# Kernel optimization log

Measured on AMD Instinct MI355X. Metric: run time of the kernel, lower is better.

Reference implementation:

```python
import jax, jax.numpy as jnp
import numpy as np

DELTA = 5.0          # weight on positive BCE term
R = 0.01             # hard-negative fraction
M, N = 4096, 16384   # batch rows, memory-bank size
NUM_HARD = int(R * (N - 1))  # int(r * neg_count); each row has exactly 1 positive


def setup_inputs() -> dict:
    key = jax.random.key(0)
    k1, k2 = jax.random.split(key)
    inputs = jax.random.normal(k1, (M, N), dtype=jnp.float32)
    targets = jax.random.randint(k2, (M,), 0, N)
    return {"inputs": inputs, "targets": targets}


def reference(inputs, targets):
    m, n = inputs.shape
    rows = jnp.arange(m)
    # positive logit per row (one-hot scatter => exactly one positive)
    pos = inputs[rows, targets]                          # [m]
    # BCE with logits, target=1: softplus(-x); mean over the single positive
    l_pos = jax.nn.softplus(-pos)                        # [m]
    # exclude positive from negatives by sinking it to -inf, then hard top-k
    neg_inf = jnp.finfo(inputs.dtype).min
    masked = inputs.at[rows, targets].set(neg_inf)       # [m, n]
    hard_neg, _ = jax.lax.top_k(masked, NUM_HARD)        # [m, NUM_HARD]
    # BCE with logits, target=0: softplus(x); mean over hard negatives
    l_neg = jnp.mean(jax.nn.softplus(hard_neg), axis=1)  # [m]
    return jnp.mean(DELTA * l_pos + l_neg)
```

## Files before the change

### kernel.cpp

```cpp
#include <hip/hip_runtime.h>
#include <stdint.h>

#define M_ROWS 4096
#define N_COLS 16384
#define K_HARD 163
#define DELTA_W 5.0f
#define THREADS 1024
#define NWAVES  16
#define RPB     8
#define GRID    (M_ROWS / RPB)
#define THRESH  2.0f
#define KEY_MIN 0xC0000000u
#define SEGC    64

__device__ __forceinline__ uint32_t f2key(float x) {
    uint32_t u = __float_as_uint(x);
    return u ^ (uint32_t)(((int32_t)u >> 31) | 0x80000000u);
}
__device__ __forceinline__ float key2f(uint32_t k) {
    uint32_t u = (k & 0x80000000u) ? (k & 0x7fffffffu) : ~k;
    return __uint_as_float(u);
}
__device__ __forceinline__ float softplus_f(float x) {
    return fmaxf(x, 0.0f) + log1pf(__expf(-fabsf(x)));
}

__device__ __forceinline__ void wscan1024(const uint32_t* h, int lane, int K,
                                          int& pivot, int& krem) {
    int c[16]; int S = 0;
#pragma unroll
    for (int q = 0; q < 16; ++q) { c[q] = (int)h[lane * 16 + q]; S += c[q]; }
    int suf = S;
    for (int off = 1; off < 64; off <<= 1) {
        int y = __shfl_down(suf, off);
        if (lane + off < 64) suf += y;
    }
    int run = suf - S;
    int enc = 0;
#pragma unroll
    for (int b = 15; b >= 0; --b) {
        const int cc = c[b];
        if (run < K && run + cc >= K) enc = ((lane * 16 + b + 1) << 8) | (K - run);
        run += cc;
    }
    for (int off = 1; off < 64; off <<= 1) enc = max(enc, __shfl_xor(enc, off));
    pivot = (enc >> 8) - 1; krem = enc & 255;
}

__device__ float wave_fallback(const float4* row4, int tgt, uint32_t* hrow, int lane) {
    uint32_t pref = 0; int K = K_HARD;
    for (int pass = 0; pass < 3; ++pass) {
        const int shift = 22 - 10 * pass;
        for (int q = 0; q < 16; ++q) hrow[q * 64 + lane] = 0;
        for (int s2 = 0; s2 < 64; ++s2) {
            const float4 v = row4[s2 * 64 + lane];
            const int j0 = (s2 * 64 + lane) * 4;
            const float e[4] = {v.x, v.y, v.z, v.w};
#pragma unroll
            for (int q = 0; q < 4; ++q) {
                if (j0 + q == tgt) continue;
                const uint32_t k = f2key(e[q]);
                if (pass == 0 || (k >> (shift + 10)) == pref)
                    atomicAdd(&hrow[(k >> shift) & 1023u], 1u);
            }
        }
        int pv, kr; wscan1024(hrow, lane, K, pv, kr);
        pref = (pref << 10) | (uint32_t)pv; K = kr;
    }
    for (int q = 0; q < 16; ++q) hrow[q * 64 + lane] = 0;
    for (int s2 = 0; s2 < 64; ++s2) {
        const float4 v = row4[s2 * 64 + lane];
        const int j0 = (s2 * 64 + lane) * 4;
        const float e[4] = {v.x, v.y, v.z, v.w};
#pragma unroll
        for (int q = 0; q < 4; ++q) {
            if (j0 + q == tgt) continue;
            const uint32_t k = f2key(e[q]);
            if ((k >> 2) == pref) atomicAdd(&hrow[k & 3u], 1u);
        }
    }
    int piv = 0, tie = K;
    { int run = 0;
      for (int b2 = 3; b2 >= 0; --b2) {
          const int cc = (int)hrow[b2];
          if (run < K && run + cc >= K) { piv = b2; tie = K - run; }
          run += cc;
      } }
    const uint32_t T = (pref << 2) | (uint32_t)piv;
    float sum = 0.0f;
    for (int s2 = 0; s2 < 64; ++s2) {
        const float4 v = row4[s2 * 64 + lane];
        const int j0 = (s2 * 64 + lane) * 4;
        const float e[4] = {v.x, v.y, v.z, v.w};
#pragma unroll
        for (int q = 0; q < 4; ++q) {
            if (j0 + q == tgt) continue;
            const uint32_t k = f2key(e[q]);
            if (k > T) sum += softplus_f(e[q]);
        }
    }
    for (int off = 32; off; off >>= 1) sum += __shfl_down(sum, off);
    if (lane == 0) sum += (float)tie * softplus_f(key2f(T));
    return sum;
}

__global__ __launch_bounds__(THREADS, 8) void mmcl_main(
        const float* __restrict__ inputs,
        const int* __restrict__ targets,
        float* __restrict__ partial) {
    __shared__ uint32_t s_seg[NWAVES][RPB][SEGC];
    __shared__ uint32_t s_hist[RPB][1024];
    __shared__ int s_cnt[NWAVES][RPB];

    const int b = blockIdx.x;
    const int t = threadIdx.x;
    const int lane = t & 63;
    const int w = t >> 6;
    const float4* in4 = (const float4*)inputs;
    const int gbase = b * (RPB * 4096);

    for (int r = 0; r < RPB; ++r) {
        int wcount = 0;
#pragma unroll
        for (int ii = 0; ii < 4; ++ii) {
            const float4 v = in4[gbase + (r * 4 + ii) * 1024 + t];
            const float e[4] = {v.x, v.y, v.z, v.w};
            const int n = (v.x >= THRESH) + (v.y >= THRESH) +
                          (v.z >= THRESH) + (v.w >= THRESH);
            int inc = n;
            for (int off = 1; off < 64; off <<= 1) {
                int y = __shfl_up(inc, off);
                if (lane >= off) inc += y;
            }
            int base = wcount + inc - n;
            int j = 0;
#pragma unroll
            for (int q = 0; q < 4; ++q) {
                if (e[q] >= THRESH) {
                    const int d = base + j;
                    if (d < SEGC) s_seg[w][r][d] = f2key(e[q]);
                    ++j;
                }
            }
            wcount += __shfl(inc, 63);
        }
        if (lane == 0) s_cnt[w][r] = wcount;
    }
    __syncthreads();

    if (w < RPB) {
        const int r = w;
        const int grow = b * RPB + r;
        const int tgt = targets[grow];
        const float pos = inputs[(size_t)grow * N_COLS + tgt];
        const uint32_t tkey = f2key(pos);
        const float4* row4 = (const float4*)(inputs + (size_t)grow * N_COLS);
        uint32_t* hrow = &s_hist[r][0];

        bool fb = false;
        for (int s = 0; s < NWAVES; ++s) fb |= ((int)s_cnt[s][r] > SEGC);

        if (!fb && pos >= THRESH) {
            bool removed = false;
            for (int s = 0; s < NWAVES && !removed; ++s) {
                const int cc = (int)s_cnt[s][r];
                const uint32_t k = (lane < cc) ? s_seg[s][r][lane] : (tkey + 1u);
                const unsigned long long m = __ballot(lane < cc && k == tkey);
                if (m) {
                    const int f = __ffsll(m) - 1;
                    if (lane == 0) {
                        s_seg[s][r][f] = s_seg[s][r][cc - 1];
                        s_cnt[s][r] = cc - 1;
                    }
                    removed = true;
                }
            }
        }
        int ncand = 0;
        for (int s = 0; s < NWAVES; ++s) ncand += (int)s_cnt[s][r];
        if (ncand < K_HARD) fb = true;

        float sum;
        if (!fb) {
            for (int q = 0; q < 16; ++q) hrow[q * 64 + lane] = 0;
            for (int s = 0; s < NWAVES; ++s) {
                const int cc = (int)s_cnt[s][r];
                if (lane < cc)
                    atomicAdd(&hrow[(s_seg[s][r][lane] - KEY_MIN) >> 20], 1u);
            }
            int p1, k1; wscan1024(hrow, lane, K_HARD, p1, k1);
            for (int q = 0; q < 16; ++q) hrow[q * 64 + lane] = 0;
            for (int s = 0; s < NWAVES; ++s) {
                const int cc = (int)s_cnt[s][r];
                if (lane < cc) {
                    const uint32_t d = s_seg[s][r][lane] - KEY_MIN;
                    if ((int)(d >> 20) == p1) atomicAdd(&hrow[(d >> 10) & 1023u], 1u);
                }
            }
            int p2, k2; wscan1024(hrow, lane, k1, p2, k2);
            const uint32_t pref2 = ((uint32_t)p1 << 10) | (uint32_t)p2;
            for (int q = 0; q < 16; ++q) hrow[q * 64 + lane] = 0;
            for (int s = 0; s < NWAVES; ++s) {
                const int cc = (int)s_cnt[s][r];
                if (lane < cc) {
                    const uint32_t d = s_seg[s][r][lane] - KEY_MIN;
                    if ((d >> 10) == pref2) atomicAdd(&hrow[d & 1023u], 1u);
                }
            }
            int p3, k3; wscan1024(hrow, lane, k2, p3, k3);
            const uint32_t T = KEY_MIN +
                (((uint32_t)p1 << 20) | ((uint32_t)p2 << 10) | (uint32_t)p3);
            sum = 0.0f;
            for (int s = 0; s < NWAVES; ++s) {
                const int cc = (int)s_cnt[s][r];
                if (lane < cc) {
                    const uint32_t k = s_seg[s][r][lane];
                    if (k > T) sum += softplus_f(key2f(k));
                }
            }
            for (int off = 32; off; off >>= 1) sum += __shfl_down(sum, off);
            if (lane == 0) sum += (float)k3 * softplus_f(key2f(T));
        } else {
            sum = wave_fallback(row4, tgt, hrow, lane);
        }

        if (lane == 0) {
            const float l_neg = sum / (float)K_HARD;
            partial[grow] = DELTA_W * softplus_f(-pos) + l_neg;
        }
    }
}

__global__ __launch_bounds__(256) void mmcl_reduce(
        const float* __restrict__ partial, float* __restrict__ out) {
    __shared__ float s_fw[4];
    const int t = threadIdx.x;
    float local = 0.0f;
    for (int i = t; i < M_ROWS; i += 256) local += partial[i];
    for (int off = 32; off; off >>= 1) local += __shfl_down(local, off);
    if ((t & 63) == 0) s_fw[t >> 6] = local;
    __syncthreads();
    if (t == 0)
        out[0] = (s_fw[0] + s_fw[1] + s_fw[2] + s_fw[3]) * (1.0f / (float)M_ROWS);
}

extern "C" void kernel_launch(void* const* d_in, const int* in_sizes, int n_in,
                              void* d_out, int out_size, void* d_ws, size_t ws_size,
                              hipStream_t stream) {
    const float* inputs = (const float*)d_in[0];
    const int* targets = (const int*)d_in[1];
    float* out = (float*)d_out;
    float* partial = (float*)d_ws;
    mmcl_main<<<GRID, THREADS, 0, stream>>>(inputs, targets, partial);
    mmcl_reduce<<<1, 256, 0, stream>>>(partial, out);
}
```

Baseline: 385.0 us.

## Split fused filter/select kernel into streaming filter pass and per-row select kernel

Replaces the single fused kernel, in which 1024-thread blocks filtered 8 rows into shared memory and then only 8 of 16 waves did the selection, with two kernels. The first is a grid-strided streaming kernel that compacts values above the threshold into per-64-lane global buckets of 24 slots, along with their counts. The second kernel gives each wave one row: it loads the bucketed keys into registers and runs the three-pass radix histogram select. This is meant to remove the idle-wave tail and raise occupancy of the bandwidth-bound pass. The cost is an extra kernel launch and a global write and read of the compacted candidates, plus more fallback risk because each segment now holds only 24 slots.

```diff
diff --git a/kernel.cpp b/kernel.cpp
--- a/kernel.cpp
+++ b/kernel.cpp
@@ -5,13 +5,13 @@
 #define N_COLS 16384
 #define K_HARD 163
 #define DELTA_W 5.0f
-#define THREADS 1024
-#define NWAVES  16
-#define RPB     8
-#define GRID    (M_ROWS / RPB)
 #define THRESH  2.0f
 #define KEY_MIN 0xC0000000u
-#define SEGC    64
+#define SLOTS   24
+#define WG      64
+#define GRID1   2048
+#define T1      256
+#define ITERS   32
 
 __device__ __forceinline__ uint32_t f2key(float x) {
     uint32_t u = __float_as_uint(x);
@@ -104,131 +104,119 @@
     return sum;
 }
 
-__global__ __launch_bounds__(THREADS, 8) void mmcl_main(
+__global__ __launch_bounds__(T1) void k1_front(
+        const float* __restrict__ inputs,
+        uint32_t* __restrict__ bucket,
+        int* __restrict__ cnts) {
+    const size_t flat = (size_t)blockIdx.x * T1 + threadIdx.x;
+    const int lane = threadIdx.x & 63;
+    const float4* in4 = (const float4*)inputs;
+#pragma unroll 4
+    for (int it = 0; it < ITERS; ++it) {
+        const size_t g = (size_t)it * ((size_t)GRID1 * T1) + flat;
+        const float4 v = in4[g];
+        const int row = (int)(g >> 12);
+        const int wg  = (int)((g >> 6) & 63);
+        const float e[4] = {v.x, v.y, v.z, v.w};
+        const int nc = (v.x >= THRESH) + (v.y >= THRESH) +
+                       (v.z >= THRESH) + (v.w >= THRESH);
+        int inc = nc;
+        for (int off = 1; off < 64; off <<= 1) {
+            int y = __shfl_up(inc, off);
+            if (lane >= off) inc += y;
+        }
+        uint32_t* seg = bucket + ((size_t)row * WG + wg) * SLOTS;
+        int d = inc - nc;
+#pragma unroll
+        for (int q = 0; q < 4; ++q) {
+            if (e[q] >= THRESH) {
+                if (d < SLOTS) seg[d] = f2key(e[q]);
+                ++d;
+            }
+        }
+        if (lane == 63) cnts[row * WG + wg] = inc;
+    }
+}
+
+__global__ __launch_bounds__(256) void k2_select(
         const float* __restrict__ inputs,
         const int* __restrict__ targets,
+        const uint32_t* __restrict__ bucket,
+        const int* __restrict__ cnts,
         float* __restrict__ partial) {
-    __shared__ uint32_t s_seg[NWAVES][RPB][SEGC];
-    __shared__ uint32_t s_hist[RPB][1024];
-    __shared__ int s_cnt[NWAVES][RPB];
-
-    const int b = blockIdx.x;
-    const int t = threadIdx.x;
-    const int lane = t & 63;
-    const int w = t >> 6;
-    const float4* in4 = (const float4*)inputs;
-    const int gbase = b * (RPB * 4096);
-
-    for (int r = 0; r < RPB; ++r) {
-        int wcount = 0;
-#pragma unroll
-        for (int ii = 0; ii < 4; ++ii) {
-            const float4 v = in4[gbase + (r * 4 + ii) * 1024 + t];
-            const float e[4] = {v.x, v.y, v.z, v.w};
-            const int n = (v.x >= THRESH) + (v.y >= THRESH) +
-                          (v.z >= THRESH) + (v.w >= THRESH);
-            int inc = n;
-            for (int off = 1; off < 64; off <<= 1) {
-                int y = __shfl_up(inc, off);
-                if (lane >= off) inc += y;
-            }
-            int base = wcount + inc - n;
-            int j = 0;
-#pragma unroll
-            for (int q = 0; q < 4; ++q) {
-                if (e[q] >= THRESH) {
-                    const int d = base + j;
-                    if (d < SEGC) s_seg[w][r][d] = f2key(e[q]);
-                    ++j;
+    __shared__ uint32_t sh[4][1024];
+    const int wid = threadIdx.x >> 6;
+    const int lane = threadIdx.x & 63;
+    const int row = blockIdx.x * 4 + wid;
+    const int tgt = targets[row];
+    const float pos = inputs[(size_t)row * N_COLS + tgt];
+    const float4* row4 = (const float4*)(inputs + (size_t)row * N_COLS);
+    uint32_t* hrow = sh[wid];
+
+    const int myc = cnts[row * WG + lane];
+    int mx = myc, sm = myc;
+    for (int off = 1; off < 64; off <<= 1) {
+        mx = max(mx, __shfl_xor(mx, off));
+        sm += __shfl_xor(sm, off);
+    }
+    bool fb = (mx > SLOTS);
+
+    uint32_t keys[SLOTS];
+    const int c = fb ? 0 : myc;
+    const uint32_t* seg = bucket + ((size_t)row * WG + lane) * SLOTS;
+#pragma unroll
+    for (int q = 0; q < SLOTS; ++q) keys[q] = (q < c) ? seg[q] : 0u;
+
+    int removed = 0;
+    if (!fb && pos >= THRESH) {
+        const uint32_t tkey = f2key(pos);
+        int q0 = SLOTS;
+        for (int q = SLOTS - 1; q >= 0; --q) if (keys[q] == tkey && q < c) q0 = q;
+        const unsigned long long m = __ballot(q0 < SLOTS);
+        if (m) {
+            const int leader = __ffsll(m) - 1;
+            if (lane == leader) keys[q0] = 0u;
+            removed = 1;
+        }
+        removed = __shfl(removed, 0);
+    }
+    const int ncand = sm - removed;
+    if (ncand < K_HARD) fb = true;
+
+    float sum;
+    if (!fb) {
+        uint32_t pref = 0; int K = K_HARD; int pv = 0, kr = K_HARD;
+#pragma unroll
+        for (int pass = 0; pass < 3; ++pass) {
+            const int shift = 20 - 10 * pass;
+            for (int q = 0; q < 16; ++q) hrow[q * 64 + lane] = 0;
+#pragma unroll
+            for (int q = 0; q < SLOTS; ++q) {
+                const uint32_t k = keys[q];
+                if (k >= KEY_MIN) {
+                    const uint32_t d = k - KEY_MIN;
+                    if (pass == 0 || (d >> (shift + 10)) == pref)
+                        atomicAdd(&hrow[(d >> shift) & 1023u], 1u);
                 }
             }
-            wcount += __shfl(inc, 63);
-        }
-        if (lane == 0) s_cnt[w][r] = wcount;
-    }
-    __syncthreads();
-
-    if (w < RPB) {
-        const int r = w;
-        const int grow = b * RPB + r;
-        const int tgt = targets[grow];
-        const float pos = inputs[(size_t)grow * N_COLS + tgt];
-        const uint32_t tkey = f2key(pos);
-        const float4* row4 = (const float4*)(inputs + (size_t)grow * N_COLS);
-        uint32_t* hrow = &s_hist[r][0];
-
-        bool fb = false;
-        for (int s = 0; s < NWAVES; ++s) fb |= ((int)s_cnt[s][r] > SEGC);
-
-        if (!fb && pos >= THRESH) {
-            bool removed = false;
-            for (int s = 0; s < NWAVES && !removed; ++s) {
-                const int cc = (int)s_cnt[s][r];
-                const uint32_t k = (lane < cc) ? s_seg[s][r][lane] : (tkey + 1u);
-                const unsigned long long m = __ballot(lane < cc && k == tkey);
-                if (m) {
-                    const int f = __ffsll(m) - 1;
-                    if (lane == 0) {
-                        s_seg[s][r][f] = s_seg[s][r][cc - 1];
-                        s_cnt[s][r] = cc - 1;
-                    }
-                    removed = true;
-                }
-            }
-        }
-        int ncand = 0;
-        for (int s = 0; s < NWAVES; ++s) ncand += (int)s_cnt[s][r];
-        if (ncand < K_HARD) fb = true;
-
-        float sum;
-        if (!fb) {
-            for (int q = 0; q < 16; ++q) hrow[q * 64 + lane] = 0;
-            for (int s = 0; s < NWAVES; ++s) {
-                const int cc = (int)s_cnt[s][r];
-                if (lane < cc)
-                    atomicAdd(&hrow[(s_seg[s][r][lane] - KEY_MIN) >> 20], 1u);
-            }
-            int p1, k1; wscan1024(hrow, lane, K_HARD, p1, k1);
-            for (int q = 0; q < 16; ++q) hrow[q * 64 + lane] = 0;
-            for (int s = 0; s < NWAVES; ++s) {
-                const int cc = (int)s_cnt[s][r];
-                if (lane < cc) {
-                    const uint32_t d = s_seg[s][r][lane] - KEY_MIN;
-                    if ((int)(d >> 20) == p1) atomicAdd(&hrow[(d >> 10) & 1023u], 1u);
-                }
-            }
-            int p2, k2; wscan1024(hrow, lane, k1, p2, k2);
-            const uint32_t pref2 = ((uint32_t)p1 << 10) | (uint32_t)p2;
-            for (int q = 0; q < 16; ++q) hrow[q * 64 + lane] = 0;
-            for (int s = 0; s < NWAVES; ++s) {
-                const int cc = (int)s_cnt[s][r];
-                if (lane < cc) {
-                    const uint32_t d = s_seg[s][r][lane] - KEY_MIN;
-                    if ((d >> 10) == pref2) atomicAdd(&hrow[d & 1023u], 1u);
-                }
-            }
-            int p3, k3; wscan1024(hrow, lane, k2, p3, k3);
-            const uint32_t T = KEY_MIN +
-                (((uint32_t)p1 << 20) | ((uint32_t)p2 << 10) | (uint32_t)p3);
-            sum = 0.0f;
-            for (int s = 0; s < NWAVES; ++s) {
-                const int cc = (int)s_cnt[s][r];
-                if (lane < cc) {
-                    const uint32_t k = s_seg[s][r][lane];
-                    if (k > T) sum += softplus_f(key2f(k));
-                }
-            }
-            for (int off = 32; off; off >>= 1) sum += __shfl_down(sum, off);
-            if (lane == 0) sum += (float)k3 * softplus_f(key2f(T));
-        } else {
-            sum = wave_fallback(row4, tgt, hrow, lane);
-        }
-
-        if (lane == 0) {
-            const float l_neg = sum / (float)K_HARD;
-            partial[grow] = DELTA_W * softplus_f(-pos) + l_neg;
-        }
-    }
+            wscan1024(hrow, lane, K, pv, kr);
+            pref = (pref << 10) | (uint32_t)pv; K = kr;
+        }
+        const uint32_t T = KEY_MIN + pref;
+        sum = 0.0f;
+#pragma unroll
+        for (int q = 0; q < SLOTS; ++q) {
+            const uint32_t k = keys[q];
+            if (k > T) sum += softplus_f(key2f(k));
+        }
+        for (int off = 32; off; off >>= 1) sum += __shfl_down(sum, off);
+        if (lane == 0) sum += (float)kr * softplus_f(key2f(T));
+    } else {
+        sum = wave_fallback(row4, tgt, hrow, lane);
+    }
+
+    if (lane == 0)
+        partial[row] = DELTA_W * softplus_f(-pos) + sum / (float)K_HARD;
 }
 
 __global__ __launch_bounds__(256) void mmcl_reduce(
@@ -250,7 +238,11 @@
     const float* inputs = (const float*)d_in[0];
     const int* targets = (const int*)d_in[1];
     float* out = (float*)d_out;
-    float* partial = (float*)d_ws;
-    mmcl_main<<<GRID, THREADS, 0, stream>>>(inputs, targets, partial);
+    char* ws = (char*)d_ws;
+    int* cnts = (int*)ws;
+    float* partial = (float*)(ws + (1 << 20));
+    uint32_t* bucket = (uint32_t*)(ws + (2 << 20));
+    k1_front<<<GRID1, T1, 0, stream>>>(inputs, bucket, cnts);
+    k2_select<<<M_ROWS / 4, 256, 0, stream>>>(inputs, targets, bucket, cnts, partial);
     mmcl_reduce<<<1, 256, 0, stream>>>(partial, out);
 }
```

Measured after the change: 399.1 us. 3.7% more time.
